# Kernel tuning notes

Hardware: AMD Instinct MI355X
Metric: run time of the kernel (lower is better)

## Reference

```python
import jax, jax.numpy as jnp
import numpy as np

B, C, T, V, D, H, KT = 64, 3, 256, 21, 128, 4, 9


def _adjacency():
    rng = np.random.default_rng(0)
    Araw = (rng.random((V, V)) < 0.3).astype(np.float32)
    Araw = np.maximum(Araw, Araw.T)
    np.fill_diagonal(Araw, 1.0)
    deg = Araw.sum(1)
    Anorm = Araw / np.sqrt(deg[:, None] * deg[None, :])  # D^-1/2 A D^-1/2
    return Araw.astype(np.float32), Anorm.astype(np.float32)


def setup_inputs() -> dict:
    key = jax.random.key(0)
    ks = jax.random.split(key, 24)
    g = lambda i, shape, sc=0.05: jax.random.normal(ks[i], shape, dtype=jnp.float32) * sc
    Araw, Anorm = _adjacency()
    return {
        'x': jax.random.normal(ks[0], (B, C, T, V), dtype=jnp.float32),
        'coord_w': g(1, (C, D)), 'coord_b': g(2, (D,)),
        'joint_emb': g(3, (V, D)),
        'graph_bias': jnp.asarray(Araw),  # nn.Parameter(A.clone().float())
        'wq': g(4, (D, D)), 'bq': g(5, (D,)),
        'wk': g(6, (D, D)), 'bk': g(7, (D,)),
        'wv': g(8, (D, D)), 'bv': g(9, (D,)),
        'wo': g(10, (D, D)), 'bo': g(11, (D,)),
        'gcn_w1': g(12, (D, D)), 'gcn_b1': g(13, (D,)),
        'tcn_w1': g(14, (D, D, KT, 1)), 'tcn_b1': g(15, (D,)),
        'gcn_w2': g(16, (D, D)), 'gcn_b2': g(17, (D,)),
        'tcn_w2': g(18, (D, D, KT, 1)), 'tcn_b2': g(19, (D,)),
        'A': jnp.asarray(Anorm),  # fixed normalized adjacency buffer
    }


def _stgcn(x, A, gw, gb, tw, tb):
    # x: [B, D, T, V]; spatial graph conv then temporal conv, residual.
    res = x
    y = jnp.einsum('bctv,vw->bctw', x, A)              # neighbor aggregation
    y = jnp.einsum('bctv,dc->bdtv', y, gw) + gb[None, :, None, None]
    y = jax.nn.relu(y)
    y = jax.lax.conv_general_dilated(
        y, tw, window_strides=(1, 1), padding=((KT // 2, KT // 2), (0, 0)),
        dimension_numbers=('NCHW', 'OIHW', 'NCHW'))     # temporal conv, kernel 9
    y = y + tb[None, :, None, None]
    return jax.nn.relu(y + res)


def reference(x, coord_w, coord_b, joint_emb, graph_bias, wq, bq, wk, bk, wv, bv,
              wo, bo, gcn_w1, gcn_b1, tcn_w1, tcn_b1, gcn_w2, gcn_b2, tcn_w2,
              tcn_b2, A):
    b, c, t, v = x.shape
    d = coord_w.shape[1]
    dh = d // H
    scale = jnp.float32(1.0 / np.sqrt(dh))
    coords = x.transpose(0, 2, 3, 1).reshape(b * t, v, c)      # [N, V, 3]
    feat = coords @ coord_w + coord_b + joint_emb              # LearnedJointEncoding
    q = (feat @ wq + bq).reshape(-1, v, H, dh)
    k = (feat @ wk + bk).reshape(-1, v, H, dh)
    val = (feat @ wv + bv).reshape(-1, v, H, dh)
    scores = jnp.einsum('nihd,njhd->nhij', q, k) * scale + graph_bias[None, None]
    attn = jax.nn.softmax(scores, axis=-1)                     # [N, H, V, V]
    out = jnp.einsum('nhij,njhd->nihd', attn, val).reshape(-1, v, d)
    feat = out @ wo + bo
    feat = feat.reshape(b, t, v, d).transpose(0, 3, 1, 2)       # [B, D, T, V]
    feat = _stgcn(feat, A, gcn_w1, gcn_b1, tcn_w1, tcn_b1)
    feat = _stgcn(feat, A, gcn_w2, gcn_b2, tcn_w2, tcn_b2)
    return feat, attn
```

## Files before the change

### kernel.cpp

```cpp
#include <hip/hip_runtime.h>
#include <hip/hip_bf16.h>

typedef __hip_bfloat16 bf16;
typedef __attribute__((ext_vector_type(8))) short short8v;
typedef __attribute__((ext_vector_type(4))) float float4v;

#define BB   64
#define CC   3
#define TLEN 256
#define VJ   21
#define DM   128
#define NH   4
#define DH   32
#define KT   9
#define NFR  (BB*TLEN)
#define MTOK (NFR*VJ)
#define NIN  22


__device__ __forceinline__ float b2f(bf16 x){ return __bfloat162float(x); }
__device__ __forceinline__ bf16  f2b(float x){ return __float2bfloat16(x); }
__device__ __forceinline__ float hb2f(short s){ return __uint_as_float(((unsigned)(unsigned short)s) << 16); }
__device__ __forceinline__ float lo16(unsigned u){ return __uint_as_float(u << 16); }
__device__ __forceinline__ float hi16(unsigned u){ return __uint_as_float(u & 0xffff0000u); }
__device__ __forceinline__ short bf2s(float x){ bf16 h = f2b(x); return *reinterpret_cast<short*>(&h); }

__global__ void detect_dtype(const void* __restrict__ xin, int nus, int* __restrict__ flag){
  const unsigned short* u = (const unsigned short*)xin;
  int lim = nus < 65536 ? nus : 65536;
  int bad = 0;
  for (int k = threadIdx.x; k < lim; k += 256){
    float f = __uint_as_float(((unsigned)u[k]) << 16);
    if (!(fabsf(f) < 1e6f)) bad = 1;
  }
  if (bad) atomicOr(flag, 1);
}

struct ConvArgs { const void* src[NIN]; int off[NIN+1]; };

__global__ void convert_inputs(ConvArgs a, bf16* __restrict__ dst,
                               const int* __restrict__ flag, int total){
  int i = blockIdx.x*256 + threadIdx.x;
  if (i >= total) return;
  bool isf32 = (*flag != 0);
  int k = 0;
  while (i >= a.off[k+1]) ++k;
  int j = i - a.off[k];
  float v;
  if (isf32) v = ((const float*)a.src[k])[j];
  else       v = __uint_as_float(((unsigned)((const unsigned short*)a.src[k])[j]) << 16);
  dst[i] = f2b(v);
}

__global__ void prep_weights(const bf16* __restrict__ wq, const bf16* __restrict__ wk,
                             const bf16* __restrict__ wv, const bf16* __restrict__ wo,
                             const bf16* __restrict__ tw1, const bf16* __restrict__ tw2,
                             bf16* __restrict__ wqT, bf16* __restrict__ wkT,
                             bf16* __restrict__ wvT, bf16* __restrict__ woT,
                             bf16* __restrict__ twT1, bf16* __restrict__ twT2){
  int i = blockIdx.x*256 + threadIdx.x;
  if (i < DM*DM){
    int d = i >> 7, e = i & 127;
    wqT[i] = wq[e*DM + d];
    wkT[i] = wk[e*DM + d];
    wvT[i] = wv[e*DM + d];
    woT[i] = wo[e*DM + d];
  }
  if (i < KT*DM*DM){
    int c = i & 127; int d = (i >> 7) & 127; int tap = i >> 14;
    twT1[i] = tw1[(d*DM + c)*KT + tap];
    twT2[i] = tw2[(d*DM + c)*KT + tap];
  }
}

__global__ __launch_bounds__(512) void qkv_gemm(const bf16* __restrict__ x,
                                                const bf16* __restrict__ cw,
                                                const bf16* __restrict__ cb,
                                                const bf16* __restrict__ je,
                                                const bf16* __restrict__ BtQ,
                                                const bf16* __restrict__ BtK,
                                                const bf16* __restrict__ BtV,
                                                const bf16* __restrict__ bq,
                                                const bf16* __restrict__ bk,
                                                const bf16* __restrict__ bv,
                                                bf16* __restrict__ Oq,
                                                bf16* __restrict__ Ok,
                                                bf16* __restrict__ Ov){
  __shared__ short8v lds[128*16];
  __shared__ float sxf[128][4];
  const int tid = threadIdx.x;
  const int r0  = blockIdx.x*128;
  const int bvi = r0 >> 8;
  const int t0  = r0 & (TLEN-1);
  const int blk_b = bvi / VJ, blk_v = bvi % VJ;
  {
    int tok = tid >> 2, c = tid & 3;
    if (tok < 128 && c < 3)
      sxf[tok][c] = b2f(x[((size_t)(blk_b*CC + c)*TLEN + t0 + tok)*VJ + blk_v]);
  }
  __syncthreads();
  for (int i = tid; i < 128*16; i += 512){
    int row = i >> 4, c0 = i & 15;
    short8v cw0 = *reinterpret_cast<const short8v*>(cw + 0*DM + c0*8);
    short8v cw1 = *reinterpret_cast<const short8v*>(cw + 1*DM + c0*8);
    short8v cw2 = *reinterpret_cast<const short8v*>(cw + 2*DM + c0*8);
    short8v cbv = *reinterpret_cast<const short8v*>(cb + c0*8);
    short8v jev = *reinterpret_cast<const short8v*>(je + blk_v*DM + c0*8);
    float x0 = sxf[row][0], x1 = sxf[row][1], x2 = sxf[row][2];
    short8v out;
    #pragma unroll
    for (int e = 0; e < 8; ++e){
      float f = hb2f(cbv[e]) + hb2f(jev[e]);
      f = fmaf(x0, hb2f(cw0[e]), f);
      f = fmaf(x1, hb2f(cw1[e]), f);
      f = fmaf(x2, hb2f(cw2[e]), f);
      out[e] = bf2s(f);
    }
    lds[row*16 + (c0 ^ (row & 7))] = out;
  }
  __syncthreads();
  const int lane = tid & 63;
  const int wid  = tid >> 6;
  const int rbase = (wid >> 2) * 64;
  const int nt0   = (wid & 3) * 2;
  const int l15 = lane & 15, l4 = lane >> 4;
  #pragma unroll
  for (int w = 0; w < 3; ++w){
    const bf16* Bt  = (w==0) ? BtQ : (w==1) ? BtK : BtV;
    const bf16* bia = (w==0) ? bq  : (w==1) ? bk  : bv;
    bf16*       Out = (w==0) ? Oq  : (w==1) ? Ok  : Ov;
    short8v breg[2][4];
    #pragma unroll
    for (int ntl = 0; ntl < 2; ++ntl)
      #pragma unroll
      for (int ks = 0; ks < 4; ++ks)
        breg[ntl][ks] = *reinterpret_cast<const short8v*>(Bt + ((nt0+ntl)*16 + l15)*DM + ks*32 + l4*8);
    float4v acc[4][2];
    #pragma unroll
    for (int rt = 0; rt < 4; ++rt){ acc[rt][0] = (float4v){0,0,0,0}; acc[rt][1] = (float4v){0,0,0,0}; }
    #pragma unroll
    for (int rt = 0; rt < 4; ++rt){
      const int ldsRow = rbase + rt*16 + l15;
      #pragma unroll
      for (int ks = 0; ks < 4; ++ks){
        short8v a = lds[ldsRow*16 + ((ks*4 + l4) ^ (ldsRow & 7))];
        acc[rt][0] = __builtin_amdgcn_mfma_f32_16x16x32_bf16(a, breg[0][ks], acc[rt][0], 0,0,0);
        acc[rt][1] = __builtin_amdgcn_mfma_f32_16x16x32_bf16(a, breg[1][ks], acc[rt][1], 0,0,0);
      }
    }
    #pragma unroll
    for (int rt = 0; rt < 4; ++rt)
      #pragma unroll
      for (int ntl = 0; ntl < 2; ++ntl){
        int col = (nt0+ntl)*16 + l15;
        float bvv = b2f(bia[col]);
        #pragma unroll
        for (int j = 0; j < 4; ++j)
          Out[(size_t)(r0 + rbase + rt*16 + l4*4 + j)*DM + col] = f2b(acc[rt][ntl][j] + bvv);
      }
  }
}

template<int NTAPS, bool RELU, bool RESID>
__global__ __launch_bounds__(256, 4) void conv_gemm(const bf16* __restrict__ A,
                                                    const bf16* __restrict__ Bt,
                                                    const bf16* __restrict__ bias,
                                                    const bf16* resid,
                                                    bf16* Cout){
  constexpr int HT   = NTAPS/2;
  constexpr int ROWS = 64 + 2*HT;
  __shared__ short8v lds[ROWS*16];
  const int tid = threadIdx.x;
  const int r0  = blockIdx.x*64;
  const int t0  = r0 & (TLEN-1);
  const long mb = r0 - t0;
  for (int i = tid; i < ROWS*16; i += 256){
    int row = i >> 4, c0 = i & 15;
    int t = t0 + row - HT;
    if (t < 0) t = 0;
    if (t > TLEN-1) t = TLEN-1;
    lds[row*16 + (c0 ^ (row & 7))] = *reinterpret_cast<const short8v*>(A + (mb + t)*DM + c0*8);
  }
  __syncthreads();
  const int lane = tid & 63;
  const int wid  = tid >> 6;
  const int nt0  = wid * 2;
  const int l15 = lane & 15, l4 = lane >> 4;
  float4v acc[4][2];
  #pragma unroll
  for (int rt = 0; rt < 4; ++rt){ acc[rt][0] = (float4v){0,0,0,0}; acc[rt][1] = (float4v){0,0,0,0}; }

  #pragma unroll
  for (int tap = 0; tap < NTAPS; ++tap){
    const bf16* Btap = Bt + (size_t)tap*DM*DM;
    short8v breg[2][4];
    #pragma unroll
    for (int ntl = 0; ntl < 2; ++ntl)
      #pragma unroll
      for (int ks = 0; ks < 4; ++ks)
        breg[ntl][ks] = *reinterpret_cast<const short8v*>(Btap + ((nt0+ntl)*16 + l15)*DM + ks*32 + l4*8);
    const int dt = tap - HT;
    #pragma unroll
    for (int rt = 0; rt < 4; ++rt){
      const int tl = rt*16 + l15;
      bool valid = true;
      if (NTAPS > 1){
        int ts = t0 + tl + dt;
        valid = (ts >= 0) && (ts < TLEN);
      }
      const int ldsRow = tl + HT + dt;
      #pragma unroll
      for (int ks = 0; ks < 4; ++ks){
        short8v a = lds[ldsRow*16 + ((ks*4 + l4) ^ (ldsRow & 7))];
        if (NTAPS > 1 && !valid) a = (short8v){0,0,0,0,0,0,0,0};
        acc[rt][0] = __builtin_amdgcn_mfma_f32_16x16x32_bf16(a, breg[0][ks], acc[rt][0], 0,0,0);
        acc[rt][1] = __builtin_amdgcn_mfma_f32_16x16x32_bf16(a, breg[1][ks], acc[rt][1], 0,0,0);
      }
    }
  }
  #pragma unroll
  for (int rt = 0; rt < 4; ++rt){
    #pragma unroll
    for (int ntl = 0; ntl < 2; ++ntl){
      int col = (nt0+ntl)*16 + l15;
      float bv = b2f(bias[col]);
      #pragma unroll
      for (int j = 0; j < 4; ++j){
        size_t idx = (size_t)(r0 + rt*16 + l4*4 + j)*DM + col;
        float val = acc[rt][ntl][j] + bv;
        if (RESID) val += b2f(resid[idx]);
        if (RELU) val = fmaxf(val, 0.f);
        Cout[idx] = f2b(val);
      }
    }
  }
}

#define POOLSZ 39936
__global__ __launch_bounds__(256) void attn_core(const bf16* __restrict__ Q,
                                                 const bf16* __restrict__ K,
                                                 const bf16* __restrict__ V,
                                                 const bf16* __restrict__ gbias,
                                                 const bf16* __restrict__ An,
                                                 const bf16* __restrict__ woT,
                                                 const bf16* __restrict__ bo,
                                                 float* __restrict__ attn_out,
                                                 bf16* __restrict__ feat_out,
                                                 bf16* __restrict__ agg_out){
  __shared__ __align__(16) char pool[POOLSZ];
  bf16*  sQ   = (bf16*) (pool + 0);
  bf16*  sK   = (bf16*) (pool + 5712);
  bf16*  sV   = (bf16*) (pool + 11424);
  float* sc   = (float*)(pool + 20128);
  bf16*  sP   = (bf16*) (pool + 27184);
  bf16*  sgb  = (bf16*) (pool + 37424);
  bf16*  sAn  = (bf16*) (pool + 38320);
  float* rmax = (float*)(pool + 39216);
  float* rinv = (float*)(pool + 39552);
  bf16*  sao  = (bf16*) (pool + 0);
  bf16*  sfeat= (bf16*) (pool + 8704);

  const int n = blockIdx.x;
  const int bb = n / TLEN, t = n % TLEN;
  const int tid = threadIdx.x;
  const int lane = tid & 63;
  const int wid  = tid >> 6;
  const int l15 = lane & 15, l4 = lane >> 4;

  for (int i = tid; i < VJ*VJ; i += 256){ sgb[i] = gbias[i]; sAn[i] = An[i]; }
  for (int i = tid; i < 2*VJ*16; i += 256){
    int c0 = i & 15; int v = (i >> 4) % VJ; int w = i / (16*VJ);
    size_t m = ((size_t)bb*VJ + v)*TLEN + t;
    const bf16* src = (w==0 ? Q : K) + m*DM + c0*8;
    bf16* dst = (w==0 ? sQ : sK) + v*136 + c0*8;
    *reinterpret_cast<short8v*>(dst) = *reinterpret_cast<const short8v*>(src);
  }
  for (int i = tid; i < 32*16; i += 256){
    int c0 = i & 15; int v = i >> 4;
    short8v val = (short8v){0,0,0,0,0,0,0,0};
    if (v < VJ){
      size_t m = ((size_t)bb*VJ + v)*TLEN + t;
      val = *reinterpret_cast<const short8v*>(V + m*DM + c0*8);
    }
    *reinterpret_cast<short8v*>(sV + v*136 + c0*8) = val;
  }
  for (int i = tid; i < 4*32*40/8; i += 256)
    reinterpret_cast<short8v*>(sP)[i] = (short8v){0,0,0,0,0,0,0,0};
  __syncthreads();

  const float scale = 0.17677669529663687f;
  {
    const int h = wid;
    short8v aq[2], bk2[2];
    #pragma unroll
    for (int mt = 0; mt < 2; ++mt){
      int i = mt*16 + l15; if (i > VJ-1) i = VJ-1;
      aq[mt] = *reinterpret_cast<const short8v*>(sQ + i*136 + h*DH + l4*8);
    }
    #pragma unroll
    for (int nt = 0; nt < 2; ++nt){
      int j = nt*16 + l15; if (j > VJ-1) j = VJ-1;
      bk2[nt] = *reinterpret_cast<const short8v*>(sK + j*136 + h*DH + l4*8);
    }
    float4v cs[2][2];
    #pragma unroll
    for (int mt = 0; mt < 2; ++mt)
      #pragma unroll
      for (int nt = 0; nt < 2; ++nt){
        cs[mt][nt] = (float4v){0,0,0,0};
        cs[mt][nt] = __builtin_amdgcn_mfma_f32_16x16x32_bf16(aq[mt], bk2[nt], cs[mt][nt], 0,0,0);
      }
    #pragma unroll
    for (int mt = 0; mt < 2; ++mt)
      #pragma unroll
      for (int nt = 0; nt < 2; ++nt){
        int j = nt*16 + l15;
        #pragma unroll
        for (int jj = 0; jj < 4; ++jj){
          int i = mt*16 + l4*4 + jj;
          if (i < VJ && j < VJ)
            sc[(h*VJ + i)*VJ + j] = cs[mt][nt][jj]*scale + b2f(sgb[i*VJ + j]);
        }
      }
  }
  __syncthreads();
  for (int r = tid; r < NH*VJ; r += 256){
    float m = -1e30f;
    for (int j = 0; j < VJ; ++j) m = fmaxf(m, sc[r*VJ + j]);
    float s = 0.f;
    for (int j = 0; j < VJ; ++j) s += __expf(sc[r*VJ + j] - m);
    rmax[r] = m; rinv[r] = 1.0f/s;
  }
  __syncthreads();
  for (int idx = tid; idx < NH*VJ*VJ; idx += 256){
    int r = idx / VJ;
    int j = idx % VJ, i2 = r % VJ, h = idx/(VJ*VJ);
    float e = __expf(sc[idx] - rmax[r]) * rinv[r];
    attn_out[(size_t)n*(NH*VJ*VJ) + idx] = e;
    sP[(h*32 + i2)*40 + j] = f2b(e);
  }
  __syncthreads();
  float4v cp[2][2];
  {
    const int h = wid;
    short8v pa[2];
    #pragma unroll
    for (int mt = 0; mt < 2; ++mt){
      int i = mt*16 + l15;
      pa[mt] = *reinterpret_cast<const short8v*>(sP + (h*32 + i)*40 + l4*8);
    }
    short8v bv2[2];
    #pragma unroll
    for (int nt = 0; nt < 2; ++nt){
      #pragma unroll
      for (int e = 0; e < 8; ++e)
        bv2[nt][e] = *reinterpret_cast<const short*>(sV + (l4*8 + e)*136 + h*DH + nt*16 + l15);
    }
    #pragma unroll
    for (int mt = 0; mt < 2; ++mt)
      #pragma unroll
      for (int nt = 0; nt < 2; ++nt){
        cp[mt][nt] = (float4v){0,0,0,0};
        cp[mt][nt] = __builtin_amdgcn_mfma_f32_16x16x32_bf16(pa[mt], bv2[nt], cp[mt][nt], 0,0,0);
      }
  }
  __syncthreads();
  for (int i = tid; i < (32-VJ)*16; i += 256){
    int row = VJ + i/16, c0 = i & 15;
    *reinterpret_cast<short8v*>(sao + row*136 + c0*8) = (short8v){0,0,0,0,0,0,0,0};
  }
  {
    const int h = wid;
    #pragma unroll
    for (int mt = 0; mt < 2; ++mt)
      #pragma unroll
      for (int nt = 0; nt < 2; ++nt){
        int d = h*DH + nt*16 + l15;
        #pragma unroll
        for (int jj = 0; jj < 4; ++jj){
          int i = mt*16 + l4*4 + jj;
          if (i < VJ) sao[i*136 + d] = f2b(cp[mt][nt][jj]);
        }
      }
  }
  __syncthreads();
  float4v acc[2][2];
  #pragma unroll
  for (int mt = 0; mt < 2; ++mt){ acc[mt][0] = (float4v){0,0,0,0}; acc[mt][1] = (float4v){0,0,0,0}; }
  #pragma unroll
  for (int ks = 0; ks < 4; ++ks){
    short8v bfr[2];
    #pragma unroll
    for (int ct = 0; ct < 2; ++ct)
      bfr[ct] = *reinterpret_cast<const short8v*>(woT + (wid*32 + ct*16 + l15)*DM + ks*32 + l4*8);
    #pragma unroll
    for (int mt = 0; mt < 2; ++mt){
      int row = mt*16 + l15;
      short8v a = *reinterpret_cast<const short8v*>(sao + row*136 + ks*32 + l4*8);
      acc[mt][0] = __builtin_amdgcn_mfma_f32_16x16x32_bf16(a, bfr[0], acc[mt][0], 0,0,0);
      acc[mt][1] = __builtin_amdgcn_mfma_f32_16x16x32_bf16(a, bfr[1], acc[mt][1], 0,0,0);
    }
  }
  #pragma unroll
  for (int mt = 0; mt < 2; ++mt){
    #pragma unroll
    for (int ct = 0; ct < 2; ++ct){
      int col = wid*32 + ct*16 + l15;
      float bov = b2f(bo[col]);
      #pragma unroll
      for (int j = 0; j < 4; ++j){
        int row = mt*16 + l4*4 + j;
        float fv = acc[mt][ct][j] + bov;
        sfeat[row*136 + col] = f2b(fv);
        if (row < VJ)
          feat_out[(((size_t)bb*VJ + row)*TLEN + t)*DM + col] = f2b(fv);
      }
    }
  }
  __syncthreads();
  float4v acg[2][2];
  #pragma unroll
  for (int mt = 0; mt < 2; ++mt){ acg[mt][0] = (float4v){0,0,0,0}; acg[mt][1] = (float4v){0,0,0,0}; }
  short8v afr[2];
  #pragma unroll
  for (int mt = 0; mt < 2; ++mt){
    int w = mt*16 + l15;
    #pragma unroll
    for (int e = 0; e < 8; ++e){
      int k = l4*8 + e;
      short vsv = 0;
      if (k < VJ && w < VJ) vsv = *reinterpret_cast<const short*>(&sAn[k*VJ + w]);
      afr[mt][e] = vsv;
    }
  }
  #pragma unroll
  for (int ct = 0; ct < 2; ++ct){
    int d = wid*32 + ct*16 + l15;
    short8v bfr;
    #pragma unroll
    for (int e = 0; e < 8; ++e){
      int k = l4*8 + e;
      bfr[e] = *reinterpret_cast<const short*>(sfeat + k*136 + d);
    }
    #pragma unroll
    for (int mt = 0; mt < 2; ++mt)
      acg[mt][ct] = __builtin_amdgcn_mfma_f32_16x16x32_bf16(afr[mt], bfr, acg[mt][ct], 0,0,0);
  }
  #pragma unroll
  for (int mt = 0; mt < 2; ++mt){
    #pragma unroll
    for (int ct = 0; ct < 2; ++ct){
      int col = wid*32 + ct*16 + l15;
      #pragma unroll
      for (int j = 0; j < 4; ++j){
        int w = mt*16 + l4*4 + j;
        if (w < VJ)
          agg_out[(((size_t)bb*VJ + w)*TLEN + t)*DM + col] = f2b(acg[mt][ct][j]);
      }
    }
  }
}

__global__ __launch_bounds__(256) void agg_kernel(const bf16* __restrict__ fin,
                                                  const bf16* __restrict__ An,
                                                  bf16* __restrict__ aout){
  const int n = blockIdx.x;
  const int bb = n / TLEN, t = n % TLEN;
  const int tid = threadIdx.x;
  __shared__ bf16 sx[VJ][136];
  __shared__ float sA[VJ*VJ];
  for (int i = tid; i < VJ*VJ; i += 256) sA[i] = b2f(An[i]);
  for (int i = tid; i < VJ*16; i += 256){
    int c0 = i & 15, v = i >> 4;
    size_t m = ((size_t)bb*VJ + v)*TLEN + t;
    *reinterpret_cast<short8v*>(&sx[v][c0*8]) =
      *reinterpret_cast<const short8v*>(fin + m*DM + c0*8);
  }
  __syncthreads();
  for (int i = tid; i < VJ*16; i += 256){
    int c0 = i & 15, w = i >> 4;
    float acc[8] = {0,0,0,0,0,0,0,0};
    #pragma unroll
    for (int u = 0; u < VJ; ++u){
      float a = sA[u*VJ + w];
      short8v xv = *reinterpret_cast<const short8v*>(&sx[u][c0*8]);
      #pragma unroll
      for (int e = 0; e < 8; ++e) acc[e] = fmaf(a, hb2f(xv[e]), acc[e]);
    }
    short8v out;
    #pragma unroll
    for (int e = 0; e < 8; ++e) out[e] = bf2s(acc[e]);
    size_t m = ((size_t)bb*VJ + w)*TLEN + t;
    *reinterpret_cast<short8v*>(aout + m*DM + c0*8) = out;
  }
}

__global__ __launch_bounds__(256) void transpose_out(const bf16* __restrict__ fin,
                                                     float* __restrict__ fout){
  const int bid = blockIdx.x;
  const int b   = bid >> 5;
  const int rem = bid & 31;
  const int t0  = (rem >> 2) * 32;
  const int d0  = (rem & 3) * 32;
  __shared__ bf16 tile[32][VJ][33];
  const int tid = threadIdx.x;
  for (int idx = tid; idx < 32*VJ*32; idx += 256){
    int dl = idx & 31;
    int v  = (idx >> 5) % VJ;
    int tl = idx / (32*VJ);
    tile[tl][v][dl] = fin[(((size_t)b*VJ + v)*TLEN + t0 + tl)*DM + d0 + dl];
  }
  __syncthreads();
  for (int idx = tid; idx < 32*VJ*32; idx += 256){
    int j  = idx % (32*VJ);
    int dl = idx / (32*VJ);
    int tl = j / VJ, v = j % VJ;
    fout[((size_t)(b*DM + d0 + dl)*TLEN + t0 + tl)*VJ + v] = b2f(tile[tl][v][dl]);
  }
}

extern "C" void kernel_launch(void* const* d_in, const int* in_sizes, int n_in,
                              void* d_out, int out_size, void* d_ws, size_t ws_size,
                              hipStream_t stream){
  const size_t featElems = (size_t)MTOK*DM;
  float* outf    = (float*)d_out;
  float* attnOut = outf + featElems;
  bf16* qbuf = (bf16*)d_out;
  bf16* kbuf = qbuf + featElems;

  char* wp = (char*)d_ws;
  auto alloc = [&](size_t bytes)->char*{ char* p = wp; wp += (bytes + 15) & ~(size_t)15; return p; };
  int*  flag = (int*)alloc(16);
  ConvArgs ca; int total = 0;
  for (int i = 0; i < NIN; ++i){ ca.src[i] = d_in[i]; ca.off[i] = total; total += in_sizes[i]; }
  ca.off[NIN] = total;
  bf16* cin   = (bf16*)alloc((size_t)total*2);
  bf16* wqT   = (bf16*)alloc(DM*DM*2);
  bf16* wkT   = (bf16*)alloc(DM*DM*2);
  bf16* wvT   = (bf16*)alloc(DM*DM*2);
  bf16* woT   = (bf16*)alloc(DM*DM*2);
  bf16* twT1  = (bf16*)alloc(KT*DM*DM*2);
  bf16* twT2  = (bf16*)alloc(KT*DM*DM*2);
  bf16* featA = (bf16*)alloc(featElems*2);
  bf16* bufV  = (bf16*)alloc(featElems*2);
  if ((size_t)(wp - (char*)d_ws) > ws_size) return;

  const bf16* x    = cin + ca.off[0];
  const bf16* cw   = cin + ca.off[1];
  const bf16* cb   = cin + ca.off[2];
  const bf16* je   = cin + ca.off[3];
  const bf16* gbias= cin + ca.off[4];
  const bf16* wq   = cin + ca.off[5];
  const bf16* bq   = cin + ca.off[6];
  const bf16* wk   = cin + ca.off[7];
  const bf16* bk   = cin + ca.off[8];
  const bf16* wv   = cin + ca.off[9];
  const bf16* bv   = cin + ca.off[10];
  const bf16* wo   = cin + ca.off[11];
  const bf16* bo   = cin + ca.off[12];
  const bf16* gw1  = cin + ca.off[13];
  const bf16* gb1  = cin + ca.off[14];
  const bf16* tw1  = cin + ca.off[15];
  const bf16* tb1  = cin + ca.off[16];
  const bf16* gw2  = cin + ca.off[17];
  const bf16* gb2  = cin + ca.off[18];
  const bf16* tw2  = cin + ca.off[19];
  const bf16* tb2  = cin + ca.off[20];
  const bf16* An   = cin + ca.off[21];

  const int GB  = MTOK/128;
  const int GB2 = MTOK/64;
  hipMemsetAsync(flag, 0, sizeof(int), stream);
  detect_dtype<<<1, 256, 0, stream>>>(d_in[0], in_sizes[0], flag);
  convert_inputs<<<(total + 255)/256, 256, 0, stream>>>(ca, cin, flag, total);
  prep_weights<<<(KT*DM*DM + 255)/256, 256, 0, stream>>>(wq, wk, wv, wo, tw1, tw2,
                                                         wqT, wkT, wvT, woT, twT1, twT2);
  qkv_gemm<<<GB, 512, 0, stream>>>(x, cw, cb, je, wqT, wkT, wvT, bq, bk, bv,
                                   qbuf, kbuf, bufV);
  attn_core<<<NFR, 256, 0, stream>>>(qbuf, kbuf, bufV, gbias, An, woT, bo,
                                     attnOut, featA, qbuf);
  conv_gemm<1,true,false><<<GB2, 256, 0, stream>>>(qbuf, gw1, gb1, nullptr, kbuf);
  conv_gemm<9,true,true><<<GB2, 256, 0, stream>>>(kbuf, twT1, tb1, featA, featA);
  agg_kernel<<<NFR, 256, 0, stream>>>(featA, An, qbuf);
  conv_gemm<1,true,false><<<GB2, 256, 0, stream>>>(qbuf, gw2, gb2, nullptr, kbuf);
  conv_gemm<9,true,true><<<GB2, 256, 0, stream>>>(kbuf, twT2, tb2, featA, featA);
  transpose_out<<<BB*(TLEN/32)*(DM/32), 256, 0, stream>>>(featA, outf);
}
```

Before: 1.181 ms.

## Fuse GCN 1x1 projection into attention and aggregation kernels

After: 1.345 ms. +13.9%, slower.

```diff
diff --git a/kernel.cpp b/kernel.cpp
--- a/kernel.cpp
+++ b/kernel.cpp
@@ -244,9 +244,11 @@
                                                  const bf16* __restrict__ An,
                                                  const bf16* __restrict__ woT,
                                                  const bf16* __restrict__ bo,
+                                                 const bf16* __restrict__ gw1,
+                                                 const bf16* __restrict__ gb1,
                                                  float* __restrict__ attn_out,
                                                  bf16* __restrict__ feat_out,
-                                                 bf16* __restrict__ agg_out){
+                                                 bf16* __restrict__ y_out){
   __shared__ __align__(16) char pool[POOLSZ];
   bf16*  sQ   = (bf16*) (pool + 0);
   bf16*  sK   = (bf16*) (pool + 5712);
@@ -259,6 +261,7 @@
   float* rinv = (float*)(pool + 39552);
   bf16*  sao  = (bf16*) (pool + 0);
   bf16*  sfeat= (bf16*) (pool + 8704);
+  bf16*  sagg = (bf16*) (pool + 27184);
 
   const int n = blockIdx.x;
   const int bb = n / TLEN, t = n % TLEN;
@@ -447,51 +450,141 @@
       acg[mt][ct] = __builtin_amdgcn_mfma_f32_16x16x32_bf16(afr[mt], bfr, acg[mt][ct], 0,0,0);
   }
   #pragma unroll
-  for (int mt = 0; mt < 2; ++mt){
+  for (int mt = 0; mt < 2; ++mt)
     #pragma unroll
     for (int ct = 0; ct < 2; ++ct){
       int col = wid*32 + ct*16 + l15;
+      #pragma unroll
+      for (int j = 0; j < 4; ++j)
+        sagg[(mt*16 + l4*4 + j)*136 + col] = f2b(acg[mt][ct][j]);
+    }
+  __syncthreads();
+  float4v acy[2][2];
+  #pragma unroll
+  for (int mt = 0; mt < 2; ++mt){ acy[mt][0] = (float4v){0,0,0,0}; acy[mt][1] = (float4v){0,0,0,0}; }
+  #pragma unroll
+  for (int ks = 0; ks < 4; ++ks){
+    short8v bfr[2];
+    #pragma unroll
+    for (int ct = 0; ct < 2; ++ct)
+      bfr[ct] = *reinterpret_cast<const short8v*>(gw1 + (wid*32 + ct*16 + l15)*DM + ks*32 + l4*8);
+    #pragma unroll
+    for (int mt = 0; mt < 2; ++mt){
+      int row = mt*16 + l15;
+      short8v a = *reinterpret_cast<const short8v*>(sagg + row*136 + ks*32 + l4*8);
+      acy[mt][0] = __builtin_amdgcn_mfma_f32_16x16x32_bf16(a, bfr[0], acy[mt][0], 0,0,0);
+      acy[mt][1] = __builtin_amdgcn_mfma_f32_16x16x32_bf16(a, bfr[1], acy[mt][1], 0,0,0);
+    }
+  }
+  #pragma unroll
+  for (int mt = 0; mt < 2; ++mt){
+    #pragma unroll
+    for (int ct = 0; ct < 2; ++ct){
+      int col = wid*32 + ct*16 + l15;
+      float gbv = b2f(gb1[col]);
       #pragma unroll
       for (int j = 0; j < 4; ++j){
         int w = mt*16 + l4*4 + j;
         if (w < VJ)
-          agg_out[(((size_t)bb*VJ + w)*TLEN + t)*DM + col] = f2b(acg[mt][ct][j]);
-      }
-    }
-  }
-}
-
-__global__ __launch_bounds__(256) void agg_kernel(const bf16* __restrict__ fin,
-                                                  const bf16* __restrict__ An,
-                                                  bf16* __restrict__ aout){
+          y_out[(((size_t)bb*VJ + w)*TLEN + t)*DM + col] = f2b(fmaxf(acy[mt][ct][j] + gbv, 0.f));
+      }
+    }
+  }
+}
+
+__global__ __launch_bounds__(256) void agg_gcn(const bf16* __restrict__ fin,
+                                               const bf16* __restrict__ An,
+                                               const bf16* __restrict__ gw,
+                                               const bf16* __restrict__ gb,
+                                               bf16* __restrict__ yout){
+  __shared__ __align__(16) bf16 sfeat[32*136];
+  __shared__ __align__(16) bf16 sagg[32*136];
+  __shared__ bf16 sAn[VJ*VJ];
   const int n = blockIdx.x;
   const int bb = n / TLEN, t = n % TLEN;
   const int tid = threadIdx.x;
-  __shared__ bf16 sx[VJ][136];
-  __shared__ float sA[VJ*VJ];
-  for (int i = tid; i < VJ*VJ; i += 256) sA[i] = b2f(An[i]);
-  for (int i = tid; i < VJ*16; i += 256){
-    int c0 = i & 15, v = i >> 4;
-    size_t m = ((size_t)bb*VJ + v)*TLEN + t;
-    *reinterpret_cast<short8v*>(&sx[v][c0*8]) =
-      *reinterpret_cast<const short8v*>(fin + m*DM + c0*8);
-  }
-  __syncthreads();
-  for (int i = tid; i < VJ*16; i += 256){
-    int c0 = i & 15, w = i >> 4;
-    float acc[8] = {0,0,0,0,0,0,0,0};
-    #pragma unroll
-    for (int u = 0; u < VJ; ++u){
-      float a = sA[u*VJ + w];
-      short8v xv = *reinterpret_cast<const short8v*>(&sx[u][c0*8]);
-      #pragma unroll
-      for (int e = 0; e < 8; ++e) acc[e] = fmaf(a, hb2f(xv[e]), acc[e]);
-    }
-    short8v out;
-    #pragma unroll
-    for (int e = 0; e < 8; ++e) out[e] = bf2s(acc[e]);
-    size_t m = ((size_t)bb*VJ + w)*TLEN + t;
-    *reinterpret_cast<short8v*>(aout + m*DM + c0*8) = out;
+  const int lane = tid & 63;
+  const int wid  = tid >> 6;
+  const int l15 = lane & 15, l4 = lane >> 4;
+  for (int i = tid; i < VJ*VJ; i += 256) sAn[i] = An[i];
+  for (int i = tid; i < 32*16; i += 256){
+    int c0 = i & 15; int v = i >> 4;
+    short8v val = (short8v){0,0,0,0,0,0,0,0};
+    if (v < VJ){
+      size_t m = ((size_t)bb*VJ + v)*TLEN + t;
+      val = *reinterpret_cast<const short8v*>(fin + m*DM + c0*8);
+    }
+    *reinterpret_cast<short8v*>(sfeat + v*136 + c0*8) = val;
+  }
+  __syncthreads();
+  float4v acg[2][2];
+  #pragma unroll
+  for (int mt = 0; mt < 2; ++mt){ acg[mt][0] = (float4v){0,0,0,0}; acg[mt][1] = (float4v){0,0,0,0}; }
+  short8v afr[2];
+  #pragma unroll
+  for (int mt = 0; mt < 2; ++mt){
+    int w = mt*16 + l15;
+    #pragma unroll
+    for (int e = 0; e < 8; ++e){
+      int k = l4*8 + e;
+      short vsv = 0;
+      if (k < VJ && w < VJ) vsv = *reinterpret_cast<const short*>(&sAn[k*VJ + w]);
+      afr[mt][e] = vsv;
+    }
+  }
+  #pragma unroll
+  for (int ct = 0; ct < 2; ++ct){
+    int d = wid*32 + ct*16 + l15;
+    short8v bfr;
+    #pragma unroll
+    for (int e = 0; e < 8; ++e){
+      int k = l4*8 + e;
+      bfr[e] = *reinterpret_cast<const short*>(sfeat + k*136 + d);
+    }
+    #pragma unroll
+    for (int mt = 0; mt < 2; ++mt)
+      acg[mt][ct] = __builtin_amdgcn_mfma_f32_16x16x32_bf16(afr[mt], bfr, acg[mt][ct], 0,0,0);
+  }
+  #pragma unroll
+  for (int mt = 0; mt < 2; ++mt)
+    #pragma unroll
+    for (int ct = 0; ct < 2; ++ct){
+      int col = wid*32 + ct*16 + l15;
+      #pragma unroll
+      for (int j = 0; j < 4; ++j)
+        sagg[(mt*16 + l4*4 + j)*136 + col] = f2b(acg[mt][ct][j]);
+    }
+  __syncthreads();
+  float4v acy[2][2];
+  #pragma unroll
+  for (int mt = 0; mt < 2; ++mt){ acy[mt][0] = (float4v){0,0,0,0}; acy[mt][1] = (float4v){0,0,0,0}; }
+  #pragma unroll
+  for (int ks = 0; ks < 4; ++ks){
+    short8v bfr[2];
+    #pragma unroll
+    for (int ct = 0; ct < 2; ++ct)
+      bfr[ct] = *reinterpret_cast<const short8v*>(gw + (wid*32 + ct*16 + l15)*DM + ks*32 + l4*8);
+    #pragma unroll
+    for (int mt = 0; mt < 2; ++mt){
+      int row = mt*16 + l15;
+      short8v a = *reinterpret_cast<const short8v*>(sagg + row*136 + ks*32 + l4*8);
+      acy[mt][0] = __builtin_amdgcn_mfma_f32_16x16x32_bf16(a, bfr[0], acy[mt][0], 0,0,0);
+      acy[mt][1] = __builtin_amdgcn_mfma_f32_16x16x32_bf16(a, bfr[1], acy[mt][1], 0,0,0);
+    }
+  }
+  #pragma unroll
+  for (int mt = 0; mt < 2; ++mt){
+    #pragma unroll
+    for (int ct = 0; ct < 2; ++ct){
+      int col = wid*32 + ct*16 + l15;
+      float gbv = b2f(gb[col]);
+      #pragma unroll
+      for (int j = 0; j < 4; ++j){
+        int w = mt*16 + l4*4 + j;
+        if (w < VJ)
+          yout[(((size_t)bb*VJ + w)*TLEN + t)*DM + col] = f2b(fmaxf(acy[mt][ct][j] + gbv, 0.f));
+      }
+    }
   }
 }
 
@@ -577,12 +670,10 @@
                                                          wqT, wkT, wvT, woT, twT1, twT2);
   qkv_gemm<<<GB, 512, 0, stream>>>(x, cw, cb, je, wqT, wkT, wvT, bq, bk, bv,
                                    qbuf, kbuf, bufV);
-  attn_core<<<NFR, 256, 0, stream>>>(qbuf, kbuf, bufV, gbias, An, woT, bo,
+  attn_core<<<NFR, 256, 0, stream>>>(qbuf, kbuf, bufV, gbias, An, woT, bo, gw1, gb1,
                                      attnOut, featA, qbuf);
-  conv_gemm<1,true,false><<<GB2, 256, 0, stream>>>(qbuf, gw1, gb1, nullptr, kbuf);
-  conv_gemm<9,true,true><<<GB2, 256, 0, stream>>>(kbuf, twT1, tb1, featA, featA);
-  agg_kernel<<<NFR, 256, 0, stream>>>(featA, An, qbuf);
-  conv_gemm<1,true,false><<<GB2, 256, 0, stream>>>(qbuf, gw2, gb2, nullptr, kbuf);
-  conv_gemm<9,true,true><<<GB2, 256, 0, stream>>>(kbuf, twT2, tb2, featA, featA);
+  conv_gemm<9,true,true><<<GB2, 256, 0, stream>>>(qbuf, twT1, tb1, featA, featA);
+  agg_gcn<<<NFR, 256, 0, stream>>>(featA, An, gw2, gb2, qbuf);
+  conv_gemm<9,true,true><<<GB2, 256, 0, stream>>>(qbuf, twT2, tb2, featA, featA);
   transpose_out<<<BB*(TLEN/32)*(DM/32), 256, 0, stream>>>(featA, outf);
 }
```
